# Kernel tuning notes

Measured on AMD Instinct MI355X. Metric: run time of the kernel, lower is better.

Reference implementation:

```python
import jax, jax.numpy as jnp
import numpy as np

M, N, K, C, G = 16384, 131072, 16, 128, 8
EPS_BN = 1e-5


def _bn(x, g, b):
    # inference-mode BatchNorm1d (running_mean=0, running_var=1)
    return x * (g / jnp.sqrt(1.0 + EPS_BN)) + b


def setup_inputs() -> dict:
    key = jax.random.key(0)
    ks = jax.random.split(key, 16)
    f32 = jnp.float32
    s = 0.05
    return {
        "query_feat": jax.random.normal(ks[0], (M, C), f32),
        "context_feat": jax.random.normal(ks[1], (N, C), f32),
        "query_coord": jax.random.normal(ks[2], (M, 3), f32),
        "context_coord": jax.random.normal(ks[3], (N, 3), f32),
        "Wq": jax.random.normal(ks[4], (C, C), f32) * s,
        "bq": jnp.zeros((C,), f32),
        "gq": jnp.ones((C,), f32),
        "betaq": jnp.zeros((C,), f32),
        "Wk": jax.random.normal(ks[5], (C, C), f32) * s,
        "bk": jnp.zeros((C,), f32),
        "gk": jnp.ones((C,), f32),
        "betak": jnp.zeros((C,), f32),
        "Wv": jax.random.normal(ks[6], (C, C), f32) * s,
        "bv": jnp.zeros((C,), f32),
        "Wp1": jax.random.normal(ks[7], (3, C), f32) * s,
        "bp1": jnp.zeros((C,), f32),
        "gp1": jnp.ones((C,), f32),
        "betap1": jnp.zeros((C,), f32),
        "Wp2": jax.random.normal(ks[8], (C, C), f32) * s,
        "bp2": jnp.zeros((C,), f32),
        "Ww1": jax.random.normal(ks[9], (C, G), f32) * s,
        "bw1": jnp.zeros((G,), f32),
        "gw1": jnp.ones((G,), f32),
        "betaw1": jnp.zeros((G,), f32),
        "Ww2": jax.random.normal(ks[10], (G, G), f32) * s,
        "bw2": jnp.zeros((G,), f32),
        "knn_indexes": jax.random.randint(ks[11], (M, K), 0, N, dtype=jnp.int32),
    }


def reference(query_feat, context_feat, query_coord, context_coord,
              Wq, bq, gq, betaq, Wk, bk, gk, betak, Wv, bv,
              Wp1, bp1, gp1, betap1, Wp2, bp2,
              Ww1, bw1, gw1, betaw1, Ww2, bw2, knn_indexes):
    q = jax.nn.relu(_bn(query_feat @ Wq + bq, gq, betaq))              # (M, C)
    k = jax.nn.relu(_bn(context_feat @ Wk + bk, gk, betak))            # (N, C)
    v = context_feat @ Wv + bv                                         # (N, C)

    mask = knn_indexes >= 0                                            # (M, K); -1 = padded neighbor
    idx = jnp.where(mask, knn_indexes, 0)
    mf = mask[..., None].astype(q.dtype)                               # (M, K, 1)

    key_g = k[idx] * mf                                                # (M, K, C) gather (zero row for -1)
    val_g = v[idx] * mf                                                # (M, K, C)
    pos = (context_coord[idx] - query_coord[:, None, :]) * mf          # (M, K, 3) relative position

    # positional-encoding bias branch (pe_bias=True, pe_multiplier=False)
    peb = jax.nn.relu(_bn(pos @ Wp1 + bp1, gp1, betap1)) @ Wp2 + bp2   # (M, K, C)
    rel = key_g - q[:, None, :] + peb                                  # (M, K, C)
    val_g = val_g + peb

    # grouped vector attention weights
    w = jax.nn.relu(_bn(rel @ Ww1 + bw1, gw1, betaw1)) @ Ww2 + bw2     # (M, K, G)
    w = jax.nn.softmax(w, axis=1) * mf                                 # softmax over neighbors, mask padded

    m_, k_ = idx.shape
    c_ = q.shape[-1]
    g_ = w.shape[-1]
    out = jnp.einsum('mkgi,mkg->mgi', val_g.reshape(m_, k_, g_, c_ // g_), w)
    return out.reshape(m_, c_)
```

## Files before the change

kernel.cpp:

```cpp
#include <hip/hip_runtime.h>

#define C 128
#define G 8
#define KNN 16
#define QB 4
#define EPS 1e-5f

typedef unsigned short u16;
typedef __attribute__((ext_vector_type(8))) short short8;
typedef __attribute__((ext_vector_type(4))) float float4v;

union frag_u { short8 v; u16 u[8]; };

__device__ inline u16 f2bf(float f) {
    unsigned u = __builtin_bit_cast(unsigned, f);
    unsigned r = (u + 0x7fffu + ((u >> 16) & 1u)) >> 16;
    return (u16)r;
}
__device__ inline float bf2f(u16 h) {
    unsigned u = ((unsigned)h) << 16;
    return __builtin_bit_cast(float, u);
}

__global__ __launch_bounds__(256) void prep_w(
    const float* __restrict__ Wk, const float* __restrict__ Wv,
    const float* __restrict__ Wq, const float* __restrict__ Wp2,
    const float* __restrict__ Ww1, u16* __restrict__ dst)
{
    const int b = blockIdx.x, t = threadIdx.x;
    if (b < 4) {
        const float* W = b == 0 ? Wk : b == 1 ? Wv : b == 2 ? Wq : Wp2;
        u16* d = dst + b * 16384;
        for (int e = t; e < 16384; e += 256) {
            const int k = e >> 7, n = e & 127;
            const int cb = n >> 4, lan = n & 15;
            const int kk = k >> 5, quad = (k >> 3) & 3, j = k & 7;
            d[(((cb * 4 + kk) * 4 + quad) * 16 + lan) * 8 + j] = f2bf(W[e]);
        }
    } else {
        u16* d = dst + 4 * 16384;
        for (int e = t; e < 4096; e += 256) {
            const int j = e & 7, lan = (e >> 3) & 15;
            const int quad = (e >> 7) & 3, kk = e >> 9;
            const int k = kk * 32 + quad * 8 + j;
            d[e] = lan < 8 ? f2bf(Ww1[k * G + lan]) : (u16)0;
        }
    }
}

template <int TWO>
__global__ __launch_bounds__(256) void proj_mfma(
    const float* __restrict__ X,
    const u16* __restrict__ PW1, const float* __restrict__ b1,
    const float* __restrict__ g1, const float* __restrict__ be1,
    const u16* __restrict__ PW2, const float* __restrict__ b2,
    u16* __restrict__ out1, u16* __restrict__ out2)
{
    __shared__ u16 Xs[64 * 136];
    const int t = threadIdx.x;
    const int w = t >> 6, l = t & 63;
    const int quad = l >> 4, lan = l & 15;
    const int row0 = blockIdx.x * 64;

    {
        const float4* Xv = (const float4*)(X + (size_t)row0 * C);
#pragma unroll
        for (int i = 0; i < 8; i++) {
            const int e = t + 256 * i;
            const int r = e >> 5, c4 = e & 31;
            const float4 f = Xv[e];
            uint2 p;
            p.x = (unsigned)f2bf(f.x) | ((unsigned)f2bf(f.y) << 16);
            p.y = (unsigned)f2bf(f.z) | ((unsigned)f2bf(f.w) << 16);
            *(uint2*)(&Xs[r * 136 + c4 * 4]) = p;
        }
    }

    short8 Bf[TWO + 1][2][4];
#pragma unroll
    for (int w2 = 0; w2 <= TWO; w2++) {
        const u16* P = w2 ? PW2 : PW1;
#pragma unroll
        for (int ct = 0; ct < 2; ct++) {
            const int cb = w * 2 + ct;
#pragma unroll
            for (int kk = 0; kk < 4; kk++)
                Bf[w2][ct][kk] = *(const short8*)(P + (((cb * 4 + kk) * 4 + quad) * 16 + lan) * 8);
        }
    }
    __syncthreads();

    float4v acc[TWO + 1][2][4];
#pragma unroll
    for (int w2 = 0; w2 <= TWO; w2++)
#pragma unroll
        for (int ct = 0; ct < 2; ct++)
#pragma unroll
            for (int rt = 0; rt < 4; rt++)
                acc[w2][ct][rt] = (float4v)0.f;

#pragma unroll
    for (int rt = 0; rt < 4; rt++) {
#pragma unroll
        for (int kk = 0; kk < 4; kk++) {
            const short8 A = *(const short8*)(&Xs[(rt * 16 + lan) * 136 + kk * 32 + quad * 8]);
#pragma unroll
            for (int w2 = 0; w2 <= TWO; w2++)
#pragma unroll
                for (int ct = 0; ct < 2; ct++)
                    acc[w2][ct][rt] = __builtin_amdgcn_mfma_f32_16x16x32_bf16(
                        A, Bf[w2][ct][kk], acc[w2][ct][rt], 0, 0, 0);
        }
    }

#pragma unroll
    for (int ct = 0; ct < 2; ct++) {
        const int cg = w * 32 + ct * 16 + lan;
        const float bb = b1[cg];
        const float sc = g1[cg] * rsqrtf(1.f + EPS);
        const float sh = be1[cg];
#pragma unroll
        for (int rt = 0; rt < 4; rt++)
#pragma unroll
            for (int reg = 0; reg < 4; reg++) {
                const int rg = row0 + rt * 16 + quad * 4 + reg;
                float y = (acc[0][ct][rt][reg] + bb) * sc + sh;
                y = y > 0.f ? y : 0.f;
                out1[(size_t)rg * C + cg] = f2bf(y);
            }
        if (TWO) {
            const float bv = b2[cg];
#pragma unroll
            for (int rt = 0; rt < 4; rt++)
#pragma unroll
                for (int reg = 0; reg < 4; reg++) {
                    const int rg = row0 + rt * 16 + quad * 4 + reg;
                    out2[(size_t)rg * C + cg] = f2bf(acc[1][ct][rt][reg] + bv);
                }
        }
    }
}

__global__ __launch_bounds__(256) void attn3(
    const u16* __restrict__ qbuf, const u16* __restrict__ kbuf,
    const u16* __restrict__ vbuf,
    const float* __restrict__ qcoord, const float* __restrict__ ccoord,
    const float* __restrict__ Wp1, const float* __restrict__ bp1,
    const float* __restrict__ gp1, const float* __restrict__ betap1,
    const u16* __restrict__ PWp2, const float* __restrict__ bp2,
    const u16* __restrict__ PWw1, const float* __restrict__ bw1,
    const float* __restrict__ gw1, const float* __restrict__ betaw1,
    const float* __restrict__ Ww2, const float* __restrict__ bw2,
    const int* __restrict__ knn, float* __restrict__ out)
{
    __shared__ u16   fA[64 * 136];
    __shared__ u16   relB[64 * 136];
    __shared__ float pxs[64], pys[64], pzs[64], mfs[64];
    __shared__ float wl[QB * 16 * G];
    __shared__ float wfin[QB * 16 * G];

    const int t = threadIdx.x;
    const int w = t >> 6, l = t & 63;
    const int quad = l >> 4, lan = l & 15;
    const int m0 = blockIdx.x * QB;

    const int rsub = t >> 4;
    const int c8 = (t & 15) * 8;
    float mfr[4];
    frag_u kg[4], vg[4];
#pragma unroll
    for (int p = 0; p < 4; p++) {
        const int ii = knn[m0 * KNN + p * 16 + rsub];
        mfr[p] = ii >= 0 ? 1.f : 0.f;
        const int i0 = ii >= 0 ? ii : 0;
        kg[p].v = *(const short8*)(kbuf + (size_t)i0 * C + c8);
        vg[p].v = *(const short8*)(vbuf + (size_t)i0 * C + c8);
    }

    if (t < 64) {
        const int q = t >> 4;
        const int ii = knn[m0 * KNN + t];
        const float mf = ii >= 0 ? 1.f : 0.f;
        const int i0 = ii >= 0 ? ii : 0;
        mfs[t] = mf;
        pxs[t] = (ccoord[i0 * 3 + 0] - qcoord[(m0 + q) * 3 + 0]) * mf;
        pys[t] = (ccoord[i0 * 3 + 1] - qcoord[(m0 + q) * 3 + 1]) * mf;
        pzs[t] = (ccoord[i0 * 3 + 2] - qcoord[(m0 + q) * 3 + 2]) * mf;
    }
    __syncthreads();

    {
        const int c = t & 127, hh = t >> 7;
        const float w0 = Wp1[c], w1_ = Wp1[C + c], w2_ = Wp1[2 * C + c];
        const float sc = gp1[c] * rsqrtf(1.f + EPS);
        const float bb = bp1[c], sh = betap1[c];
#pragma unroll
        for (int r2 = 0; r2 < 32; r2++) {
            const int r = hh * 32 + r2;
            float y = fmaf(pxs[r], w0, fmaf(pys[r], w1_, fmaf(pzs[r], w2_, bb)));
            y = y * sc + sh;
            y = y > 0.f ? y : 0.f;
            fA[r * 136 + c] = f2bf(y);
        }
    }
    __syncthreads();

    {
        short8 Bf[2][4];
#pragma unroll
        for (int ct = 0; ct < 2; ct++) {
            const int cb = w * 2 + ct;
#pragma unroll
            for (int kk = 0; kk < 4; kk++)
                Bf[ct][kk] = *(const short8*)(PWp2 + (((cb * 4 + kk) * 4 + quad) * 16 + lan) * 8);
        }
        float4v acc[2][4];
#pragma unroll
        for (int ct = 0; ct < 2; ct++)
#pragma unroll
            for (int q = 0; q < 4; q++) acc[ct][q] = (float4v)0.f;

#pragma unroll
        for (int q = 0; q < 4; q++) {
#pragma unroll
            for (int kk = 0; kk < 4; kk++) {
                const short8 A = *(const short8*)(&fA[(q * 16 + lan) * 136 + kk * 32 + quad * 8]);
#pragma unroll
                for (int ct = 0; ct < 2; ct++)
                    acc[ct][q] = __builtin_amdgcn_mfma_f32_16x16x32_bf16(
                        A, Bf[ct][kk], acc[ct][q], 0, 0, 0);
            }
        }
        const float bb0 = bp2[w * 32 + lan];
        const float bb1 = bp2[w * 32 + 16 + lan];
#pragma unroll
        for (int ct = 0; ct < 2; ct++)
#pragma unroll
            for (int q = 0; q < 4; q++)
#pragma unroll
                for (int reg = 0; reg < 4; reg++)
                    relB[(q * 16 + quad * 4 + reg) * 136 + w * 32 + ct * 16 + lan] =
                        f2bf(acc[ct][q][reg] + (ct ? bb1 : bb0));
    }
    __syncthreads();

    {
#pragma unroll
        for (int p = 0; p < 4; p++) {
            const int r = p * 16 + rsub;
            const float mf = mfr[p];
            frag_u qg, peb, relv, valv;
            qg.v  = *(const short8*)(qbuf + (size_t)(m0 + p) * C + c8);
            peb.v = *(const short8*)(&relB[r * 136 + c8]);
#pragma unroll
            for (int j = 0; j < 8; j++) {
                const float pe = bf2f(peb.u[j]);
                relv.u[j] = f2bf(fmaf(bf2f(kg[p].u[j]), mf, pe - bf2f(qg.u[j])));
                valv.u[j] = f2bf(fmaf(bf2f(vg[p].u[j]), mf, pe));
            }
            *(short8*)(&relB[r * 136 + c8]) = relv.v;
            *(short8*)(&fA[r * 136 + c8])  = valv.v;
        }
    }
    __syncthreads();

    {
        short8 Bw[4];
#pragma unroll
        for (int kk = 0; kk < 4; kk++)
            Bw[kk] = *(const short8*)(PWw1 + ((kk * 4 + quad) * 16 + lan) * 8);
        float4v acc = (float4v)0.f;
#pragma unroll
        for (int kk = 0; kk < 4; kk++) {
            const short8 A = *(const short8*)(&relB[(w * 16 + lan) * 136 + kk * 32 + quad * 8]);
            acc = __builtin_amdgcn_mfma_f32_16x16x32_bf16(A, Bw[kk], acc, 0, 0, 0);
        }
        if (lan < G) {
            const int g = lan;
            const float sc = gw1[g] * rsqrtf(1.f + EPS);
            const float bb = bw1[g], sh = betaw1[g];
#pragma unroll
            for (int reg = 0; reg < 4; reg++) {
                const int j = quad * 4 + reg;
                float y = (acc[reg] + bb) * sc + sh;
                wl[w * 128 + j * 8 + g] = y > 0.f ? y : 0.f;
            }
        }
    }
    __syncthreads();

    if (t < QB * G) {
        const int q = t >> 3, g2 = t & 7;
        float w2c[G];
#pragma unroll
        for (int g = 0; g < G; g++) w2c[g] = Ww2[g * G + g2];
        const float bb = bw2[g2];
        float lg[KNN], mx = -1e30f;
#pragma unroll
        for (int j = 0; j < KNN; j++) {
            float a = bb;
#pragma unroll
            for (int g = 0; g < G; g++) a = fmaf(wl[q * 128 + j * 8 + g], w2c[g], a);
            lg[j] = a;
            mx = fmaxf(mx, a);
        }
        float sum = 0.f;
#pragma unroll
        for (int j = 0; j < KNN; j++) { lg[j] = __expf(lg[j] - mx); sum += lg[j]; }
        const float inv = 1.f / sum;
#pragma unroll
        for (int j = 0; j < KNN; j++)
            wfin[q * 128 + j * 8 + g2] = lg[j] * inv * mfs[q * 16 + j];
    }
    __syncthreads();

#pragma unroll
    for (int i = 0; i < 2; i++) {
        const int e = t + 256 * i;
        const int q = e >> 7, c = e & 127, g = c >> 4;
        float a = 0.f;
#pragma unroll
        for (int j = 0; j < KNN; j++)
            a = fmaf(bf2f(fA[(q * 16 + j) * 136 + c]), wfin[q * 128 + j * 8 + g], a);
        out[(size_t)(m0 + q) * C + c] = a;
    }
}

extern "C" void kernel_launch(void* const* d_in, const int* in_sizes, int n_in,
                              void* d_out, int out_size, void* d_ws, size_t ws_size,
                              hipStream_t stream)
{
    const float* query_feat    = (const float*)d_in[0];
    const float* context_feat  = (const float*)d_in[1];
    const float* query_coord   = (const float*)d_in[2];
    const float* context_coord = (const float*)d_in[3];
    const float* Wq    = (const float*)d_in[4];
    const float* bq    = (const float*)d_in[5];
    const float* gq    = (const float*)d_in[6];
    const float* betaq = (const float*)d_in[7];
    const float* Wk    = (const float*)d_in[8];
    const float* bk    = (const float*)d_in[9];
    const float* gk    = (const float*)d_in[10];
    const float* betak = (const float*)d_in[11];
    const float* Wv    = (const float*)d_in[12];
    const float* bv    = (const float*)d_in[13];
    const float* Wp1   = (const float*)d_in[14];
    const float* bp1   = (const float*)d_in[15];
    const float* gp1   = (const float*)d_in[16];
    const float* betap1= (const float*)d_in[17];
    const float* Wp2   = (const float*)d_in[18];
    const float* bp2   = (const float*)d_in[19];
    const float* Ww1   = (const float*)d_in[20];
    const float* bw1   = (const float*)d_in[21];
    const float* gw1   = (const float*)d_in[22];
    const float* betaw1= (const float*)d_in[23];
    const float* Ww2   = (const float*)d_in[24];
    const float* bw2   = (const float*)d_in[25];
    const int*   knn   = (const int*)d_in[26];

    const int M = in_sizes[0] / C;
    const int N = in_sizes[1] / C;

    u16* kb = (u16*)d_ws;
    u16* vb = kb + (size_t)N * C;
    u16* qb = vb + (size_t)N * C;
    u16* pw = qb + (size_t)M * C;
    u16* pWk  = pw;
    u16* pWv  = pw + 16384;
    u16* pWq  = pw + 2 * 16384;
    u16* pWp2 = pw + 3 * 16384;
    u16* pWw1 = pw + 4 * 16384;

    prep_w<<<5, 256, 0, stream>>>(Wk, Wv, Wq, Wp2, Ww1, pw);
    proj_mfma<1><<<N / 64, 256, 0, stream>>>(context_feat, pWk, bk, gk, betak,
                                             pWv, bv, kb, vb);
    proj_mfma<0><<<M / 64, 256, 0, stream>>>(query_feat, pWq, bq, gq, betaq,
                                             nullptr, nullptr, qb, nullptr);
    attn3<<<M / QB, 256, 0, stream>>>(qb, kb, vb, query_coord, context_coord,
                                      Wp1, bp1, gp1, betap1, pWp2, bp2,
                                      pWw1, bw1, gw1, betaw1, Ww2, bw2,
                                      knn, (float*)d_out);
}
```

Before: 236.3 us.

## Fuse query projection into attention kernel and stage K/V stores through LDS

Result: slower. 244.6 us (+3.5%).

```diff
diff --git a/kernel.cpp b/kernel.cpp
--- a/kernel.cpp
+++ b/kernel.cpp
@@ -48,22 +48,22 @@
     }
 }
 
-template <int TWO>
-__global__ __launch_bounds__(256) void proj_mfma(
+__global__ __launch_bounds__(256) void proj_kv(
     const float* __restrict__ X,
-    const u16* __restrict__ PW1, const float* __restrict__ b1,
-    const float* __restrict__ g1, const float* __restrict__ be1,
-    const u16* __restrict__ PW2, const float* __restrict__ b2,
-    u16* __restrict__ out1, u16* __restrict__ out2)
+    const u16* __restrict__ PWk, const float* __restrict__ bk,
+    const float* __restrict__ gk, const float* __restrict__ betak,
+    const u16* __restrict__ PWv, const float* __restrict__ bv,
+    u16* __restrict__ kout, u16* __restrict__ vout)
 {
     __shared__ u16 Xs[64 * 136];
+    __shared__ u16 Os[64 * 136];
     const int t = threadIdx.x;
     const int w = t >> 6, l = t & 63;
     const int quad = l >> 4, lan = l & 15;
-    const int row0 = blockIdx.x * 64;
-
-    {
-        const float4* Xv = (const float4*)(X + (size_t)row0 * C);
+    const long long row0 = (long long)blockIdx.x * 64;
+
+    {
+        const float4* Xv = (const float4*)(X + row0 * C);
 #pragma unroll
         for (int i = 0; i < 8; i++) {
             const int e = t + 256 * i;
@@ -76,10 +76,10 @@
         }
     }
 
-    short8 Bf[TWO + 1][2][4];
-#pragma unroll
-    for (int w2 = 0; w2 <= TWO; w2++) {
-        const u16* P = w2 ? PW2 : PW1;
+    short8 Bf[2][2][4];
+#pragma unroll
+    for (int w2 = 0; w2 < 2; w2++) {
+        const u16* P = w2 ? PWv : PWk;
 #pragma unroll
         for (int ct = 0; ct < 2; ct++) {
             const int cb = w * 2 + ct;
@@ -90,9 +90,9 @@
     }
     __syncthreads();
 
-    float4v acc[TWO + 1][2][4];
-#pragma unroll
-    for (int w2 = 0; w2 <= TWO; w2++)
+    float4v acc[2][2][4];
+#pragma unroll
+    for (int w2 = 0; w2 < 2; w2++)
 #pragma unroll
         for (int ct = 0; ct < 2; ct++)
 #pragma unroll
@@ -105,7 +105,7 @@
         for (int kk = 0; kk < 4; kk++) {
             const short8 A = *(const short8*)(&Xs[(rt * 16 + lan) * 136 + kk * 32 + quad * 8]);
 #pragma unroll
-            for (int w2 = 0; w2 <= TWO; w2++)
+            for (int w2 = 0; w2 < 2; w2++)
 #pragma unroll
                 for (int ct = 0; ct < 2; ct++)
                     acc[w2][ct][rt] = __builtin_amdgcn_mfma_f32_16x16x32_bf16(
@@ -116,35 +116,52 @@
 #pragma unroll
     for (int ct = 0; ct < 2; ct++) {
         const int cg = w * 32 + ct * 16 + lan;
-        const float bb = b1[cg];
-        const float sc = g1[cg] * rsqrtf(1.f + EPS);
-        const float sh = be1[cg];
+        const float bb = bk[cg];
+        const float sc = gk[cg] * rsqrtf(1.f + EPS);
+        const float sh = betak[cg];
 #pragma unroll
         for (int rt = 0; rt < 4; rt++)
 #pragma unroll
             for (int reg = 0; reg < 4; reg++) {
-                const int rg = row0 + rt * 16 + quad * 4 + reg;
                 float y = (acc[0][ct][rt][reg] + bb) * sc + sh;
                 y = y > 0.f ? y : 0.f;
-                out1[(size_t)rg * C + cg] = f2bf(y);
+                Os[(rt * 16 + quad * 4 + reg) * 136 + cg] = f2bf(y);
             }
-        if (TWO) {
-            const float bv = b2[cg];
-#pragma unroll
-            for (int rt = 0; rt < 4; rt++)
-#pragma unroll
-                for (int reg = 0; reg < 4; reg++) {
-                    const int rg = row0 + rt * 16 + quad * 4 + reg;
-                    out2[(size_t)rg * C + cg] = f2bf(acc[1][ct][rt][reg] + bv);
-                }
-        }
-    }
-}
-
-__global__ __launch_bounds__(256) void attn3(
-    const u16* __restrict__ qbuf, const u16* __restrict__ kbuf,
-    const u16* __restrict__ vbuf,
+    }
+    __syncthreads();
+#pragma unroll
+    for (int i = 0; i < 4; i++) {
+        const int e = t + 256 * i;
+        const int r = e >> 4, cc = (e & 15) * 8;
+        *(short8*)(kout + (row0 + r) * C + cc) = *(const short8*)(&Os[r * 136 + cc]);
+    }
+    __syncthreads();
+
+#pragma unroll
+    for (int ct = 0; ct < 2; ct++) {
+        const int cg = w * 32 + ct * 16 + lan;
+        const float bb = bv[cg];
+#pragma unroll
+        for (int rt = 0; rt < 4; rt++)
+#pragma unroll
+            for (int reg = 0; reg < 4; reg++)
+                Os[(rt * 16 + quad * 4 + reg) * 136 + cg] = f2bf(acc[1][ct][rt][reg] + bb);
+    }
+    __syncthreads();
+#pragma unroll
+    for (int i = 0; i < 4; i++) {
+        const int e = t + 256 * i;
+        const int r = e >> 4, cc = (e & 15) * 8;
+        *(short8*)(vout + (row0 + r) * C + cc) = *(const short8*)(&Os[r * 136 + cc]);
+    }
+}
+
+__global__ __launch_bounds__(256) void attn4(
+    const float* __restrict__ qfeat,
+    const u16* __restrict__ kbuf, const u16* __restrict__ vbuf,
     const float* __restrict__ qcoord, const float* __restrict__ ccoord,
+    const u16* __restrict__ PWq, const float* __restrict__ bq,
+    const float* __restrict__ gq, const float* __restrict__ betaq,
     const float* __restrict__ Wp1, const float* __restrict__ bp1,
     const float* __restrict__ gp1, const float* __restrict__ betap1,
     const u16* __restrict__ PWp2, const float* __restrict__ bp2,
@@ -155,9 +172,9 @@
 {
     __shared__ u16   fA[64 * 136];
     __shared__ u16   relB[64 * 136];
+    __shared__ float qs[QB * C];
     __shared__ float pxs[64], pys[64], pzs[64], mfs[64];
     __shared__ float wl[QB * 16 * G];
-    __shared__ float wfin[QB * 16 * G];
 
     const int t = threadIdx.x;
     const int w = t >> 6, l = t & 63;
@@ -177,6 +194,20 @@
         vg[p].v = *(const short8*)(vbuf + (size_t)i0 * C + c8);
     }
 
+    {
+        frag_u z;
+        if (rsub < QB) {
+            const float4 f0 = *(const float4*)(qfeat + (size_t)(m0 + rsub) * C + c8);
+            const float4 f1 = *(const float4*)(qfeat + (size_t)(m0 + rsub) * C + c8 + 4);
+            z.u[0] = f2bf(f0.x); z.u[1] = f2bf(f0.y);
+            z.u[2] = f2bf(f0.z); z.u[3] = f2bf(f0.w);
+            z.u[4] = f2bf(f1.x); z.u[5] = f2bf(f1.y);
+            z.u[6] = f2bf(f1.z); z.u[7] = f2bf(f1.w);
+        } else {
+            z.v = (short8)0;
+        }
+        *(short8*)(&relB[rsub * 136 + c8]) = z.v;
+    }
     if (t < 64) {
         const int q = t >> 4;
         const int ii = knn[m0 * KNN + t];
@@ -190,6 +221,40 @@
     __syncthreads();
 
     {
+        short8 Bq[2][4];
+#pragma unroll
+        for (int ct = 0; ct < 2; ct++) {
+            const int cb = w * 2 + ct;
+#pragma unroll
+            for (int kk = 0; kk < 4; kk++)
+                Bq[ct][kk] = *(const short8*)(PWq + (((cb * 4 + kk) * 4 + quad) * 16 + lan) * 8);
+        }
+        float4v aq[2];
+        aq[0] = (float4v)0.f; aq[1] = (float4v)0.f;
+#pragma unroll
+        for (int kk = 0; kk < 4; kk++) {
+            const short8 A = *(const short8*)(&relB[lan * 136 + kk * 32 + quad * 8]);
+#pragma unroll
+            for (int ct = 0; ct < 2; ct++)
+                aq[ct] = __builtin_amdgcn_mfma_f32_16x16x32_bf16(A, Bq[ct][kk], aq[ct], 0, 0, 0);
+        }
+        if (quad == 0) {
+#pragma unroll
+            for (int ct = 0; ct < 2; ct++) {
+                const int col = w * 32 + ct * 16 + lan;
+                const float bb = bq[col];
+                const float sc = gq[col] * rsqrtf(1.f + EPS);
+                const float sh = betaq[col];
+#pragma unroll
+                for (int reg = 0; reg < 4; reg++) {
+                    float y = (aq[ct][reg] + bb) * sc + sh;
+                    qs[reg * C + col] = y > 0.f ? y : 0.f;
+                }
+            }
+        }
+    }
+
+    {
         const int c = t & 127, hh = t >> 7;
         const float w0 = Wp1[c], w1_ = Wp1[C + c], w2_ = Wp1[2 * C + c];
         const float sc = gp1[c] * rsqrtf(1.f + EPS);
@@ -249,13 +314,13 @@
         for (int p = 0; p < 4; p++) {
             const int r = p * 16 + rsub;
             const float mf = mfr[p];
-            frag_u qg, peb, relv, valv;
-            qg.v  = *(const short8*)(qbuf + (size_t)(m0 + p) * C + c8);
+            frag_u peb, relv, valv;
             peb.v = *(const short8*)(&relB[r * 136 + c8]);
 #pragma unroll
             for (int j = 0; j < 8; j++) {
                 const float pe = bf2f(peb.u[j]);
-                relv.u[j] = f2bf(fmaf(bf2f(kg[p].u[j]), mf, pe - bf2f(qg.u[j])));
+                const float qv = qs[p * C + c8 + j];
+                relv.u[j] = f2bf(fmaf(bf2f(kg[p].u[j]), mf, pe - qv));
                 valv.u[j] = f2bf(fmaf(bf2f(vg[p].u[j]), mf, pe));
             }
             *(short8*)(&relB[r * 136 + c8]) = relv.v;
@@ -310,7 +375,7 @@
         const float inv = 1.f / sum;
 #pragma unroll
         for (int j = 0; j < KNN; j++)
-            wfin[q * 128 + j * 8 + g2] = lg[j] * inv * mfs[q * 16 + j];
+            wl[q * 128 + j * 8 + g2] = lg[j] * inv * mfs[q * 16 + j];
     }
     __syncthreads();
 
@@ -321,7 +386,7 @@
         float a = 0.f;
 #pragma unroll
         for (int j = 0; j < KNN; j++)
-            a = fmaf(bf2f(fA[(q * 16 + j) * 136 + c]), wfin[q * 128 + j * 8 + g], a);
+            a = fmaf(bf2f(fA[(q * 16 + j) * 136 + c]), wl[q * 128 + j * 8 + g], a);
         out[(size_t)(m0 + q) * C + c] = a;
     }
 }
@@ -363,8 +428,7 @@
 
     u16* kb = (u16*)d_ws;
     u16* vb = kb + (size_t)N * C;
-    u16* qb = vb + (size_t)N * C;
-    u16* pw = qb + (size_t)M * C;
+    u16* pw = vb + (size_t)N * C;
     u16* pWk  = pw;
     u16* pWv  = pw + 16384;
     u16* pWq  = pw + 2 * 16384;
@@ -372,11 +436,10 @@
     u16* pWw1 = pw + 4 * 16384;
 
     prep_w<<<5, 256, 0, stream>>>(Wk, Wv, Wq, Wp2, Ww1, pw);
-    proj_mfma<1><<<N / 64, 256, 0, stream>>>(context_feat, pWk, bk, gk, betak,
-                                             pWv, bv, kb, vb);
-    proj_mfma<0><<<M / 64, 256, 0, stream>>>(query_feat, pWq, bq, gq, betaq,
-                                             nullptr, nullptr, qb, nullptr);
-    attn3<<<M / QB, 256, 0, stream>>>(qb, kb, vb, query_coord, context_coord,
+    proj_kv<<<N / 64, 256, 0, stream>>>(context_feat, pWk, bk, gk, betak,
+                                        pWv, bv, kb, vb);
+    attn4<<<M / QB, 256, 0, stream>>>(query_feat, kb, vb, query_coord, context_coord,
+                                      pWq, bq, gq, betaq,
                                       Wp1, bp1, gp1, betap1, pWp2, bp2,
                                       pWw1, bw1, gw1, betaw1, Ww2, bw2,
                                       knn, (float*)d_out);
```
